# Performance work log

Measured on AMD Instinct MI355X. Metric: run time of the kernel, lower is better.

Reference implementation:

```python
import jax, jax.numpy as jnp
import numpy as np

H = 256           # hidden_size
D_IN = 4 * H      # 1024
D_K = 8 * H       # 2048
B, N = 8, 2048


def setup_inputs() -> dict:
    key = jax.random.key(0)
    ks = jax.random.split(key, 7)
    s_in = 1.0 / np.sqrt(D_IN)
    s_dk = 1.0 / np.sqrt(D_K)
    x = jax.random.normal(ks[0], (B, N, D_IN), dtype=jnp.float32)
    Wq = jax.random.uniform(ks[1], (D_IN, D_K), jnp.float32, -s_in, s_in)
    Wk = jax.random.uniform(ks[2], (D_IN, D_K), jnp.float32, -s_in, s_in)
    Wv = jax.random.uniform(ks[3], (D_IN, D_K), jnp.float32, -s_in, s_in)
    Wfc = jax.random.uniform(ks[4], (D_K, D_IN), jnp.float32, -s_dk, s_dk)
    bfc = jax.random.uniform(ks[5], (D_IN,), jnp.float32, -s_dk, s_dk)
    gamma = jnp.ones((D_IN,), jnp.float32)
    beta = jnp.zeros((D_IN,), jnp.float32)
    return {"x": x, "Wq": Wq, "Wk": Wk, "Wv": Wv, "Wfc": Wfc,
            "bfc": bfc, "gamma": gamma, "beta": beta}


def layer_norm(y, gamma, beta, eps=1e-5):
    mu = jnp.mean(y, axis=-1, keepdims=True)
    var = jnp.var(y, axis=-1, keepdims=True)
    return (y - mu) * jax.lax.rsqrt(var + eps) * gamma + beta


def reference(x, Wq, Wk, Wv, Wfc, bfc, gamma, beta):
    # Q/K/V projections: [B, N, D_K]
    q = jnp.einsum('bnd,dk->bnk', x, Wq)
    k = jnp.einsum('bnd,dk->bnk', x, Wk)
    v = jnp.einsum('bnd,dk->bnk', x, Wv)
    # NOTE: original module has NO 1/sqrt(d_k) scaling — keep it faithful.
    scores = jnp.einsum('bnk,bmk->bnm', q, k)           # [B, N, N]
    attn = jax.nn.softmax(scores, axis=-1)
    att_x = jnp.einsum('bnm,bmk->bnk', attn, v)          # [B, N, D_K]
    h = jax.nn.relu(jnp.einsum('bnk,kd->bnd', att_x, Wfc) + bfc)
    return layer_norm(x + h, gamma, beta)
```

## Files before the change

kernel.cpp:

```cpp
#include <hip/hip_runtime.h>
#include <stdint.h>


#define DEVI __device__ __forceinline__

typedef uint16_t u16;
typedef _Float16 f16x8 __attribute__((ext_vector_type(8)));
typedef float f32x4 __attribute__((ext_vector_type(4)));

DEVI u16 f2h(float f) {
  union { _Float16 h; u16 u; } v;
  v.h = (_Float16)f;
  return v.u;
}
DEVI float h2f(u16 x) {
  union { _Float16 h; u16 u; } v;
  v.u = x;
  return (float)v.h;
}

DEVI void gload_lds16(const void* g, void* lds) {
  __builtin_amdgcn_global_load_lds(
      (const __attribute__((address_space(1))) void*)g,
      (__attribute__((address_space(3))) void*)lds, 16, 0, 0);
}

#define GATE_S(N) do { asm volatile("s_waitcnt vmcnt(" #N ")" ::: "memory"); \
                       __builtin_amdgcn_s_barrier(); } while (0)
#define LGKM0 do { asm volatile("s_waitcnt lgkmcnt(0)" ::: "memory"); \
                   __builtin_amdgcn_sched_barrier(0); } while (0)

template <int EPI>
__global__ __launch_bounds__(512, 2) void gemm8x(
    const u16* __restrict__ A, const u16* __restrict__ B, void* __restrict__ C,
    int K, int lda, int ldb, int ldc,
    long aZ, long bZ, long cZ,
    const float* __restrict__ bias, const float* __restrict__ xres)
{
  __shared__ u16 lds[EPI == 3 ? 256 * 264 : 2 * 32768];
  char* ldsB = (char*)lds;
  const int tid = threadIdx.x;
  const int bz = blockIdx.z;

  const int gx = gridDim.x;
  int fl = blockIdx.y * gx + blockIdx.x;
  const int cpx = (gx * gridDim.y) >> 3;
  fl = (fl & 7) * cpx + (fl >> 3);
  const int bx = fl % gx, by = fl / gx;

  const u16* Ab = A + (long)bz * aZ + (long)(by * 256) * lda;
  const u16* Bb = B + (long)bz * bZ + (long)(bx * 256) * ldb;

  const int wid = tid >> 6, lane = tid & 63;
  const int wm = wid >> 2, wn = wid & 3;
  const int l15 = lane & 15;

  int aBase[2][2]; long aoff[2][2];
  int bBase[2][2]; long boff[2][2];
#pragma unroll
  for (int h = 0; h < 2; ++h) {
#pragma unroll
    for (int j = 0; j < 2; ++j) {
      const int s = wid * 2 + j;
      int rs = (s < 8) ? (64 * h + s * 8) : (128 + 64 * h + (s - 8) * 8);
      aBase[h][j] = rs * 128;
      {
        const int d = rs * 128 + lane * 16;
        const int dl = d ^ (((d >> 7) & 7) << 4);
        aoff[h][j] = (long)(dl >> 7) * (lda * 2) + (dl & 127);
      }
      rs = 64 * (s >> 2) + 32 * h + (s & 3) * 8;
      bBase[h][j] = 32768 + rs * 128;
      {
        const int d = rs * 128 + lane * 16;
        const int dl = d ^ (((d >> 7) & 7) << 4);
        boff[h][j] = (long)(dl >> 7) * (ldb * 2) + (dl & 127);
      }
    }
  }

  const int swz = (lane & 7) << 4;
  const int ko0 = ((lane >> 4) * 16) ^ swz;
  const int ko1 = (64 + (lane >> 4) * 16) ^ swz;

  f32x4 acc[8][4] = {};

  auto STAGE_A = [&](int t, int h) {
    char* dst = ldsB + (t & 1) * 65536;
    const long kB = (long)t * 128;
#pragma unroll
    for (int j = 0; j < 2; ++j)
      gload_lds16((const char*)Ab + aoff[h][j] + kB, dst + aBase[h][j]);
  };
  auto STAGE_B = [&](int t, int h) {
    char* dst = ldsB + (t & 1) * 65536;
    const long kB = (long)t * 128;
#pragma unroll
    for (int j = 0; j < 2; ++j)
      gload_lds16((const char*)Bb + boff[h][j] + kB, dst + bBase[h][j]);
  };
  auto RD_A = [&](const char* base, int mh, f16x8* dst) {
#pragma unroll
    for (int m = 0; m < 4; ++m) {
      const char* r = base + (wm * 128 + (mh * 4 + m) * 16 + l15) * 128;
      dst[2 * m] = *(const f16x8*)(r + ko0);
      dst[2 * m + 1] = *(const f16x8*)(r + ko1);
    }
  };
  auto RD_B = [&](const char* base, int nh, f16x8* dst) {
#pragma unroll
    for (int n = 0; n < 2; ++n) {
      const char* r = base + 32768 + (wn * 64 + (nh * 2 + n) * 16 + l15) * 128;
      dst[2 * n] = *(const f16x8*)(r + ko0);
      dst[2 * n + 1] = *(const f16x8*)(r + ko1);
    }
  };

  const int NT = K >> 6;
  const int NI = NT >> 1;
  const char* buf0 = ldsB;
  const char* buf1 = ldsB + 65536;

  STAGE_A(0, 0); STAGE_B(0, 0); STAGE_B(0, 1); STAGE_A(0, 1);
  STAGE_A(1, 0); STAGE_B(1, 0); STAGE_B(1, 1);

  for (int i = 0; i < NI; ++i) {
    const bool last = (i + 1 == NI);
    const int ta = 2 * i, tb = 2 * i + 1;
    f16x8 af[8], b0v[4], b1v[4];

    GATE_S(10);
    RD_A(buf0, 0, af); RD_B(buf0, 0, b0v);
    STAGE_A(tb, 1);
    LGKM0;
    __builtin_amdgcn_s_setprio(1);
#pragma unroll
    for (int ks = 0; ks < 2; ++ks)
#pragma unroll
      for (int m = 0; m < 4; ++m)
#pragma unroll
        for (int n = 0; n < 2; ++n)
          acc[m][n] = __builtin_amdgcn_mfma_f32_16x16x32_f16(
              af[2 * m + ks], b0v[2 * n + ks], acc[m][n], 0, 0, 0);
    __builtin_amdgcn_s_setprio(0);

    GATE_S(10);
    RD_B(buf0, 1, b1v);
    if (!last) STAGE_A(ta + 2, 0);
    LGKM0;
    __builtin_amdgcn_s_setprio(1);
#pragma unroll
    for (int ks = 0; ks < 2; ++ks)
#pragma unroll
      for (int m = 0; m < 4; ++m)
#pragma unroll
        for (int n = 0; n < 2; ++n)
          acc[m][n + 2] = __builtin_amdgcn_mfma_f32_16x16x32_f16(
              af[2 * m + ks], b1v[2 * n + ks], acc[m][n + 2], 0, 0, 0);
    __builtin_amdgcn_s_setprio(0);

    if (!last) GATE_S(10); else GATE_S(8);
    RD_A(buf0, 1, af);
    if (!last) STAGE_B(ta + 2, 0);
    LGKM0;
    __builtin_amdgcn_s_setprio(1);
#pragma unroll
    for (int ks = 0; ks < 2; ++ks)
#pragma unroll
      for (int m = 0; m < 4; ++m)
#pragma unroll
        for (int n = 0; n < 2; ++n)
          acc[m + 4][n] = __builtin_amdgcn_mfma_f32_16x16x32_f16(
              af[2 * m + ks], b0v[2 * n + ks], acc[m + 4][n], 0, 0, 0);
    __builtin_amdgcn_s_setprio(0);

    __builtin_amdgcn_s_barrier();
    if (!last) STAGE_B(ta + 2, 1);
    __builtin_amdgcn_s_setprio(1);
#pragma unroll
    for (int ks = 0; ks < 2; ++ks)
#pragma unroll
      for (int m = 0; m < 4; ++m)
#pragma unroll
        for (int n = 0; n < 2; ++n)
          acc[m + 4][n + 2] = __builtin_amdgcn_mfma_f32_16x16x32_f16(
              af[2 * m + ks], b1v[2 * n + ks], acc[m + 4][n + 2], 0, 0, 0);
    __builtin_amdgcn_s_setprio(0);

    if (!last) GATE_S(10); else GATE_S(4);
    RD_A(buf1, 0, af); RD_B(buf1, 0, b0v);
    if (!last) STAGE_A(ta + 2, 1);
    LGKM0;
    __builtin_amdgcn_s_setprio(1);
#pragma unroll
    for (int ks = 0; ks < 2; ++ks)
#pragma unroll
      for (int m = 0; m < 4; ++m)
#pragma unroll
        for (int n = 0; n < 2; ++n)
          acc[m][n] = __builtin_amdgcn_mfma_f32_16x16x32_f16(
              af[2 * m + ks], b0v[2 * n + ks], acc[m][n], 0, 0, 0);
    __builtin_amdgcn_s_setprio(0);

    if (!last) GATE_S(10); else GATE_S(2);
    RD_B(buf1, 1, b1v);
    if (!last) STAGE_A(tb + 2, 0);
    LGKM0;
    __builtin_amdgcn_s_setprio(1);
#pragma unroll
    for (int ks = 0; ks < 2; ++ks)
#pragma unroll
      for (int m = 0; m < 4; ++m)
#pragma unroll
        for (int n = 0; n < 2; ++n)
          acc[m][n + 2] = __builtin_amdgcn_mfma_f32_16x16x32_f16(
              af[2 * m + ks], b1v[2 * n + ks], acc[m][n + 2], 0, 0, 0);
    __builtin_amdgcn_s_setprio(0);

    if (!last) GATE_S(10); else GATE_S(0);
    RD_A(buf1, 1, af);
    if (!last) STAGE_B(tb + 2, 0);
    LGKM0;
    __builtin_amdgcn_s_setprio(1);
#pragma unroll
    for (int ks = 0; ks < 2; ++ks)
#pragma unroll
      for (int m = 0; m < 4; ++m)
#pragma unroll
        for (int n = 0; n < 2; ++n)
          acc[m + 4][n] = __builtin_amdgcn_mfma_f32_16x16x32_f16(
              af[2 * m + ks], b0v[2 * n + ks], acc[m + 4][n], 0, 0, 0);
    __builtin_amdgcn_s_setprio(0);

    __builtin_amdgcn_s_barrier();
    if (!last) STAGE_B(tb + 2, 1);
    __builtin_amdgcn_s_setprio(1);
#pragma unroll
    for (int ks = 0; ks < 2; ++ks)
#pragma unroll
      for (int m = 0; m < 4; ++m)
#pragma unroll
        for (int n = 0; n < 2; ++n)
          acc[m + 4][n + 2] = __builtin_amdgcn_mfma_f32_16x16x32_f16(
              af[2 * m + ks], b1v[2 * n + ks], acc[m + 4][n + 2], 0, 0, 0);
    __builtin_amdgcn_s_setprio(0);
  }

  const long cBase = (long)bz * cZ;
  const int rowBase = by * 256 + wm * 128;
  const int colBase = bx * 256 + wn * 64;

  if constexpr (EPI == 3) {
    u16* ldsT = (u16*)ldsB;
#pragma unroll
    for (int m = 0; m < 8; ++m) {
      const int row0 = wm * 128 + m * 16 + (lane >> 4) * 4;
#pragma unroll
      for (int n = 0; n < 4; ++n) {
        const int colL = wn * 64 + n * 16 + l15;
        ushort4 h;
        h.x = f2h(acc[m][n][0]); h.y = f2h(acc[m][n][1]);
        h.z = f2h(acc[m][n][2]); h.w = f2h(acc[m][n][3]);
        *(ushort4*)(ldsT + colL * 264 + row0) = h;
      }
    }
    __syncthreads();
    u16* vT = (u16*)C;
    const int rowBlk = by * 256;
    const long base2 = ((long)rowBlk >> 11) * 4194304L + (rowBlk & 2047);
#pragma unroll
    for (int p = 0; p < 16; ++p) {
      const int idx = tid + p * 512;
      const int colL = idx >> 5;
      const int ch = idx & 31;
      uint4 v = *(const uint4*)(ldsT + colL * 264 + ch * 8);
      *(uint4*)(vT + base2 + (long)(bx * 256 + colL) * 2048 + ch * 8) = v;
    }
  } else {
#pragma unroll
    for (int m = 0; m < 8; ++m) {
#pragma unroll
      for (int r = 0; r < 4; ++r) {
        const long row = rowBase + m * 16 + (lane >> 4) * 4 + r;
#pragma unroll
        for (int n = 0; n < 4; ++n) {
          const int col = colBase + n * 16 + l15;
          float v = acc[m][n][r];
          if constexpr (EPI == 0) {
            ((u16*)C)[cBase + row * ldc + col] = f2h(v);
          } else {
            v += bias[col];
            v = fmaxf(v, 0.0f);
            v += xres[row * (long)ldc + col];
            ((float*)C)[row * (long)ldc + col] = v;
          }
        }
      }
    }
  }
}

template <int EPI>
__global__ __launch_bounds__(256) void gemm_bt(
    const u16* __restrict__ A, const u16* __restrict__ B, void* __restrict__ C,
    int K, int lda, int ldb, int ldc,
    long aZ, long bZ, long cZ,
    const float* __restrict__ bias, const float* __restrict__ xres)
{
  __shared__ u16 sA[128 * 32];
  __shared__ u16 sB[128 * 32];
  const int tid = threadIdx.x;
  const int bz = blockIdx.z;
  const u16* Ab = A + (long)bz * aZ + (long)(blockIdx.y * 128) * lda;
  const u16* Bb = B + (long)bz * bZ + (long)(blockIdx.x * 128) * ldb;

  const int lane = tid & 63;
  const int wr = (tid >> 7) & 1;
  const int wc = (tid >> 6) & 1;
  const int l15 = lane & 15, l4 = lane >> 4;

  const int f0 = tid, f1 = tid + 256;
  const long ga0 = (long)(f0 >> 2) * lda + (f0 & 3) * 8;
  const long ga1 = (long)(f1 >> 2) * lda + (f1 & 3) * 8;
  const long gb0 = (long)(f0 >> 2) * ldb + (f0 & 3) * 8;
  const long gb1 = (long)(f1 >> 2) * ldb + (f1 & 3) * 8;
  u16* sAd0 = sA + (tid & ~63) * 8;
  u16* sAd1 = sA + 2048 + (tid & ~63) * 8;
  u16* sBd0 = sB + (tid & ~63) * 8;
  u16* sBd1 = sB + 2048 + (tid & ~63) * 8;

  f32x4 acc[4][4] = {};

  for (int k0 = 0; k0 < K; k0 += 32) {
    gload_lds16(Ab + ga0 + k0, sAd0);
    gload_lds16(Ab + ga1 + k0, sAd1);
    gload_lds16(Bb + gb0 + k0, sBd0);
    gload_lds16(Bb + gb1 + k0, sBd1);
    __syncthreads();
    f16x8 af[4], bf[4];
#pragma unroll
    for (int m = 0; m < 4; ++m)
      af[m] = *(const f16x8*)(sA + (wr * 64 + m * 16 + l15) * 32 + l4 * 8);
#pragma unroll
    for (int n = 0; n < 4; ++n)
      bf[n] = *(const f16x8*)(sB + (wc * 64 + n * 16 + l15) * 32 + l4 * 8);
#pragma unroll
    for (int m = 0; m < 4; ++m)
#pragma unroll
      for (int n = 0; n < 4; ++n)
        acc[m][n] = __builtin_amdgcn_mfma_f32_16x16x32_f16(af[m], bf[n], acc[m][n], 0, 0, 0);
    __syncthreads();
  }

  const long cBase = (long)bz * cZ;
  const int rowBase = blockIdx.y * 128 + wr * 64;
  const int colBase = blockIdx.x * 128 + wc * 64;

#pragma unroll
  for (int m = 0; m < 4; ++m) {
#pragma unroll
    for (int r = 0; r < 4; ++r) {
      const long row = rowBase + m * 16 + l4 * 4 + r;
#pragma unroll
      for (int n = 0; n < 4; ++n) {
        const int col = colBase + n * 16 + l15;
        float v = acc[m][n][r];
        if constexpr (EPI == 0) {
          ((u16*)C)[cBase + row * ldc + col] = f2h(v);
        } else if constexpr (EPI == 1) {
          ((float*)C)[cBase + row * ldc + col] = v;
        } else {
          v += bias[col];
          v = fmaxf(v, 0.0f);
          v += xres[row * (long)ldc + col];
          ((float*)C)[row * (long)ldc + col] = v;
        }
      }
    }
  }
}

__global__ __launch_bounds__(256) void softmax_rows16(u16* __restrict__ sc)
{
  const long row = blockIdx.x;
  u16* p = sc + row * 2048;
  const int tid = threadIdx.x;
  uint4 w = ((const uint4*)p)[tid];
  float e[8];
  e[0] = h2f(w.x & 0xffff); e[1] = h2f(w.x >> 16);
  e[2] = h2f(w.y & 0xffff); e[3] = h2f(w.y >> 16);
  e[4] = h2f(w.z & 0xffff); e[5] = h2f(w.z >> 16);
  e[6] = h2f(w.w & 0xffff); e[7] = h2f(w.w >> 16);
  float m = fmaxf(fmaxf(fmaxf(e[0], e[1]), fmaxf(e[2], e[3])),
                  fmaxf(fmaxf(e[4], e[5]), fmaxf(e[6], e[7])));
#pragma unroll
  for (int o = 32; o; o >>= 1) m = fmaxf(m, __shfl_xor(m, o));
  __shared__ float redm[4];
  if ((tid & 63) == 0) redm[tid >> 6] = m;
  __syncthreads();
  m = fmaxf(fmaxf(redm[0], redm[1]), fmaxf(redm[2], redm[3]));

  float s = 0.0f;
#pragma unroll
  for (int i = 0; i < 8; ++i) { e[i] = __expf(e[i] - m); s += e[i]; }
#pragma unroll
  for (int o = 32; o; o >>= 1) s += __shfl_xor(s, o);
  __shared__ float reds[4];
  if ((tid & 63) == 0) reds[tid >> 6] = s;
  __syncthreads();
  s = (reds[0] + reds[1]) + (reds[2] + reds[3]);
  const float inv = 1.0f / s;

  uint4 o;
  o.x = (uint32_t)f2h(e[0] * inv) | ((uint32_t)f2h(e[1] * inv) << 16);
  o.y = (uint32_t)f2h(e[2] * inv) | ((uint32_t)f2h(e[3] * inv) << 16);
  o.z = (uint32_t)f2h(e[4] * inv) | ((uint32_t)f2h(e[5] * inv) << 16);
  o.w = (uint32_t)f2h(e[6] * inv) | ((uint32_t)f2h(e[7] * inv) << 16);
  ((uint4*)p)[tid] = o;
}

__global__ __launch_bounds__(256) void softmax_rows(float* __restrict__ scores)
{
  const long row = blockIdx.x;
  const float* src = scores + row * 2048;
  const int tid = threadIdx.x;
  float4 a = ((const float4*)src)[tid];
  float4 b = ((const float4*)src)[tid + 256];
  float m = fmaxf(fmaxf(fmaxf(a.x, a.y), fmaxf(a.z, a.w)),
                  fmaxf(fmaxf(b.x, b.y), fmaxf(b.z, b.w)));
#pragma unroll
  for (int o = 32; o; o >>= 1) m = fmaxf(m, __shfl_xor(m, o));
  __shared__ float redm[4];
  if ((tid & 63) == 0) redm[tid >> 6] = m;
  __syncthreads();
  m = fmaxf(fmaxf(redm[0], redm[1]), fmaxf(redm[2], redm[3]));

  float e[8];
  e[0] = __expf(a.x - m); e[1] = __expf(a.y - m);
  e[2] = __expf(a.z - m); e[3] = __expf(a.w - m);
  e[4] = __expf(b.x - m); e[5] = __expf(b.y - m);
  e[6] = __expf(b.z - m); e[7] = __expf(b.w - m);
  float s = ((e[0] + e[1]) + (e[2] + e[3])) + ((e[4] + e[5]) + (e[6] + e[7]));
#pragma unroll
  for (int o = 32; o; o >>= 1) s += __shfl_xor(s, o);
  __shared__ float reds[4];
  if ((tid & 63) == 0) reds[tid >> 6] = s;
  __syncthreads();
  s = (reds[0] + reds[1]) + (reds[2] + reds[3]);
  const float inv = 1.0f / s;

  u16* dst = (u16*)scores + row * 4096;
  uint2 w0, w1;
  w0.x = (uint32_t)f2h(e[0] * inv) | ((uint32_t)f2h(e[1] * inv) << 16);
  w0.y = (uint32_t)f2h(e[2] * inv) | ((uint32_t)f2h(e[3] * inv) << 16);
  w1.x = (uint32_t)f2h(e[4] * inv) | ((uint32_t)f2h(e[5] * inv) << 16);
  w1.y = (uint32_t)f2h(e[6] * inv) | ((uint32_t)f2h(e[7] * inv) << 16);
  ((uint2*)dst)[tid] = w0;
  ((uint2*)dst)[tid + 256] = w1;
}

__global__ __launch_bounds__(256) void layernorm_rows(
    const float* __restrict__ y, const float* __restrict__ gamma,
    const float* __restrict__ beta, float* __restrict__ out)
{
  const long row = blockIdx.x;
  const int tid = threadIdx.x;
  float4 v = ((const float4*)(y + row * 1024))[tid];
  float s = (v.x + v.y) + (v.z + v.w);
  float q = (v.x * v.x + v.y * v.y) + (v.z * v.z + v.w * v.w);
#pragma unroll
  for (int o = 32; o; o >>= 1) { s += __shfl_xor(s, o); q += __shfl_xor(q, o); }
  __shared__ float rs[4], rq[4];
  if ((tid & 63) == 0) { rs[tid >> 6] = s; rq[tid >> 6] = q; }
  __syncthreads();
  s = (rs[0] + rs[1]) + (rs[2] + rs[3]);
  q = (rq[0] + rq[1]) + (rq[2] + rq[3]);
  const float mu = s * (1.0f / 1024.0f);
  const float var = q * (1.0f / 1024.0f) - mu * mu;
  const float rstd = rsqrtf(var + 1e-5f);
  float4 g = ((const float4*)gamma)[tid];
  float4 be = ((const float4*)beta)[tid];
  float4 o;
  o.x = (v.x - mu) * rstd * g.x + be.x;
  o.y = (v.y - mu) * rstd * g.y + be.y;
  o.z = (v.z - mu) * rstd * g.z + be.z;
  o.w = (v.w - mu) * rstd * g.w + be.w;
  __syncthreads();
  ((float4*)(out + row * 1024))[tid] = o;
}

__global__ __launch_bounds__(256) void cvt_f32_f16(
    const float* __restrict__ in, u16* __restrict__ out, long n4)
{
  const long stride = (long)gridDim.x * 256;
  for (long i = (long)blockIdx.x * 256 + threadIdx.x; i < n4; i += stride) {
    float4 v = ((const float4*)in)[i];
    uint2 p;
    p.x = (uint32_t)f2h(v.x) | ((uint32_t)f2h(v.y) << 16);
    p.y = (uint32_t)f2h(v.z) | ((uint32_t)f2h(v.w) << 16);
    ((uint2*)out)[i] = p;
  }
}

__global__ __launch_bounds__(256) void tw_f32(
    const float* __restrict__ in, u16* __restrict__ out, int R, int C)
{
  __shared__ float T[32][33];
  const int c0 = blockIdx.x * 32, r0 = blockIdx.y * 32;
  const int tx = threadIdx.x & 31, ty = threadIdx.x >> 5;
#pragma unroll
  for (int i = 0; i < 4; ++i)
    T[ty + i * 8][tx] = in[(long)(r0 + ty + i * 8) * C + c0 + tx];
  __syncthreads();
#pragma unroll
  for (int i = 0; i < 4; ++i)
    out[(long)(c0 + ty + i * 8) * R + r0 + tx] = f2h(T[tx][ty + i * 8]);
}

__global__ __launch_bounds__(256) void transpose_u16(
    const u16* __restrict__ in, u16* __restrict__ out, int R, int C)
{
  __shared__ u16 T[32][33];
  const long zo = (long)blockIdx.z * R * C;
  const int c0 = blockIdx.x * 32, r0 = blockIdx.y * 32;
  const int tx = threadIdx.x & 31, ty = threadIdx.x >> 5;
#pragma unroll
  for (int i = 0; i < 4; ++i)
    T[ty + i * 8][tx] = in[zo + (long)(r0 + ty + i * 8) * C + c0 + tx];
  __syncthreads();
#pragma unroll
  for (int i = 0; i < 4; ++i)
    out[zo + (long)(c0 + ty + i * 8) * R + r0 + tx] = T[tx][ty + i * 8];
}

extern "C" void kernel_launch(void* const* d_in, const int* in_sizes, int n_in,
                              void* d_out, int out_size, void* d_ws, size_t ws_size,
                              hipStream_t stream)
{
  const float* x     = (const float*)d_in[0];
  const float* Wq    = (const float*)d_in[1];
  const float* Wk    = (const float*)d_in[2];
  const float* Wv    = (const float*)d_in[3];
  const float* Wfc   = (const float*)d_in[4];
  const float* bfc   = (const float*)d_in[5];
  const float* gamma = (const float*)d_in[6];
  const float* beta  = (const float*)d_in[7];
  float* out = (float*)d_out;

  char* ws = (char*)d_ws;

  u16* wqkvT = (u16*)(ws + 0);
  u16* wfcT  = (u16*)(ws + 12582912);
  tw_f32<<<dim3(64, 32), 256, 0, stream>>>(Wq, wqkvT, 1024, 2048);
  tw_f32<<<dim3(64, 32), 256, 0, stream>>>(Wk, wqkvT + (long)2048 * 1024, 1024, 2048);
  tw_f32<<<dim3(64, 32), 256, 0, stream>>>(Wv, wqkvT + (long)2 * 2048 * 1024, 1024, 2048);
  tw_f32<<<dim3(32, 64), 256, 0, stream>>>(Wfc, wfcT, 2048, 1024);

  if (ws_size >= 251658240ULL) {
    u16*  q_   = (u16*)(ws + 16777216);
    u16*  k_   = (u16*)(ws + 83886080);
    u16*  vT   = (u16*)(ws + 150994944);
    u16*  sc16 = (u16*)(ws + 218103808);
    u16*  xb   = sc16;

    cvt_f32_f16<<<2048, 256, 0, stream>>>(x, xb, (long)16384 * 1024 / 4);

    gemm8x<0><<<dim3(8, 64, 2), 512, 0, stream>>>(
        xb, wqkvT, (void*)q_, 1024, 1024, 1024, 2048,
        0L, (long)2048 * 1024, (long)16384 * 2048, nullptr, nullptr);
    gemm8x<3><<<dim3(8, 64, 1), 512, 0, stream>>>(
        xb, wqkvT + (long)2 * 2048 * 1024, (void*)vT, 1024, 1024, 1024, 2048,
        0L, 0L, 0L, nullptr, nullptr);

    for (int c = 0; c < 2; ++c) {
      const u16* qc = q_ + (long)c * 1024 * 2048;
      gemm8x<0><<<dim3(8, 4, 8), 512, 0, stream>>>(
          qc, k_, (void*)sc16, 2048, 2048, 2048, 2048,
          (long)2048 * 2048, (long)2048 * 2048, (long)1024 * 2048, nullptr, nullptr);
      softmax_rows16<<<8192, 256, 0, stream>>>(sc16);
      gemm8x<0><<<dim3(8, 4, 8), 512, 0, stream>>>(
          sc16, vT, (void*)(q_ + (long)c * 1024 * 2048), 2048, 2048, 2048, 2048,
          (long)1024 * 2048, (long)2048 * 2048, (long)2048 * 2048, nullptr, nullptr);
    }

    gemm8x<2><<<dim3(4, 64, 1), 512, 0, stream>>>(
        q_, wfcT, (void*)out, 2048, 2048, 2048, 1024,
        0L, 0L, 0L, bfc, x);
  } else if (ws_size >= 109051904ULL) {
    u16*  xb2 = (u16*)(ws + 16777216);
    u16*  q2  = (u16*)(ws + 25165824);
    u16*  k2  = q2 + (long)2 * 2048 * 2048;
    u16*  v2  = q2 + (long)4 * 2048 * 2048;
    float* sc2 = (float*)(ws + 75497472);
    u16*  vT2   = k2;
    u16*  attx2 = q2;

    for (int p = 0; p < 4; ++p) {
      const float* xp = x + (long)p * 4096 * 1024;
      cvt_f32_f16<<<1024, 256, 0, stream>>>(xp, xb2, (long)4096 * 1024 / 4);
      for (int b = 0; b < 2; ++b)
        gemm_bt<0><<<dim3(16, 16, 3), 256, 0, stream>>>(
            xb2 + (long)b * 2048 * 1024, wqkvT, (void*)(q2 + (long)b * 2048 * 2048),
            1024, 1024, 1024, 2048,
            0L, (long)2048 * 1024, (long)2 * 2048 * 2048, nullptr, nullptr);
      gemm_bt<1><<<dim3(16, 16, 2), 256, 0, stream>>>(
          q2, k2, (void*)sc2, 2048, 2048, 2048, 2048,
          (long)2048 * 2048, (long)2048 * 2048, (long)2048 * 2048, nullptr, nullptr);
      softmax_rows<<<4096, 256, 0, stream>>>(sc2);
      transpose_u16<<<dim3(64, 64, 2), 256, 0, stream>>>(v2, vT2, 2048, 2048);
      gemm_bt<0><<<dim3(16, 16, 2), 256, 0, stream>>>(
          (const u16*)sc2, vT2, (void*)attx2, 2048, 4096, 2048, 2048,
          (long)2048 * 4096, (long)2048 * 2048, (long)2048 * 2048, nullptr, nullptr);
      gemm_bt<2><<<dim3(8, 32, 1), 256, 0, stream>>>(
          attx2, wfcT, (void*)(out + (long)p * 4096 * 1024), 2048, 2048, 2048, 1024,
          0L, 0L, 0L, bfc, xp);
    }
  } else {
    u16*  xb_b   = (u16*)(ws + 16777216);
    u16*  qkv_b  = (u16*)(ws + 20971520);
    u16*  q_b    = qkv_b;
    u16*  k_b    = qkv_b + (long)2048 * 2048;
    u16*  v_b    = qkv_b + (long)2 * 2048 * 2048;
    float* sc_b  = (float*)(ws + 46137344);
    u16*  vT_b   = k_b;
    u16*  attx_b = q_b;

    for (int b = 0; b < 8; ++b) {
      const float* x_b = x + (long)b * 2048 * 1024;
      cvt_f32_f16<<<512, 256, 0, stream>>>(x_b, xb_b, (long)2048 * 1024 / 4);
      gemm_bt<0><<<dim3(16, 16, 3), 256, 0, stream>>>(
          xb_b, wqkvT, (void*)qkv_b, 1024, 1024, 1024, 2048,
          0L, (long)2048 * 1024, (long)2048 * 2048, nullptr, nullptr);
      gemm_bt<1><<<dim3(16, 16, 1), 256, 0, stream>>>(
          q_b, k_b, (void*)sc_b, 2048, 2048, 2048, 2048,
          0L, 0L, 0L, nullptr, nullptr);
      softmax_rows<<<2048, 256, 0, stream>>>(sc_b);
      transpose_u16<<<dim3(64, 64, 1), 256, 0, stream>>>(v_b, vT_b, 2048, 2048);
      gemm_bt<0><<<dim3(16, 16, 1), 256, 0, stream>>>(
          (const u16*)sc_b, vT_b, (void*)attx_b, 2048, 4096, 2048, 2048,
          0L, 0L, 0L, nullptr, nullptr);
      gemm_bt<2><<<dim3(8, 16, 1), 256, 0, stream>>>(
          attx_b, wfcT, (void*)(out + (long)b * 2048 * 1024), 2048, 2048, 2048, 1024,
          0L, 0L, 0L, bfc, x_b);
    }
  }

  layernorm_rows<<<16384, 256, 0, stream>>>(out, gamma, beta, out);
}
```

Measured before the change: 592.2 us.

## Restructure GEMM main-loop sync: per-buffer vmcnt waits with split barriers

Replaces the per-quadrant combined vmcnt-wait-plus-barrier gates with a single vmcnt wait per half-iteration (per LDS buffer) and extra barriers placed around each MFMA quadrant. The aim is to stop stalling on outstanding global-to-LDS loads before every quadrant and to let loads overlap longer with compute. The cost is more barriers per iteration. It also risks racing on LDS reuse if the reduced vmcnt gating does not fully cover the data each quadrant reads. MFMA blocks are folded into a macro with no functional change.

```diff
diff --git a/kernel.cpp b/kernel.cpp
--- a/kernel.cpp
+++ b/kernel.cpp
@@ -25,10 +25,10 @@
       (__attribute__((address_space(3))) void*)lds, 16, 0, 0);
 }
 
-#define GATE_S(N) do { asm volatile("s_waitcnt vmcnt(" #N ")" ::: "memory"); \
-                       __builtin_amdgcn_s_barrier(); } while (0)
 #define LGKM0 do { asm volatile("s_waitcnt lgkmcnt(0)" ::: "memory"); \
                    __builtin_amdgcn_sched_barrier(0); } while (0)
+#define VMC(N) asm volatile("s_waitcnt vmcnt(" #N ")" ::: "memory")
+#define BAR()  __builtin_amdgcn_s_barrier()
 
 template <int EPI>
 __global__ __launch_bounds__(512, 2) void gemm8x(
@@ -116,6 +116,18 @@
     }
   };
 
+#define MFMA_QUAD(MO, NO, AV, BV)                                        \
+  __builtin_amdgcn_s_setprio(1);                                         \
+  _Pragma("unroll")                                                      \
+  for (int ks = 0; ks < 2; ++ks)                                         \
+    _Pragma("unroll")                                                    \
+    for (int m = 0; m < 4; ++m)                                          \
+      _Pragma("unroll")                                                  \
+      for (int n = 0; n < 2; ++n)                                        \
+        acc[m + MO][n + NO] = __builtin_amdgcn_mfma_f32_16x16x32_f16(    \
+            AV[2 * m + ks], BV[2 * n + ks], acc[m + MO][n + NO], 0, 0, 0); \
+  __builtin_amdgcn_s_setprio(0)
+
   const int NT = K >> 6;
   const int NI = NT >> 1;
   const char* buf0 = ldsB;
@@ -123,128 +135,69 @@
 
   STAGE_A(0, 0); STAGE_B(0, 0); STAGE_B(0, 1); STAGE_A(0, 1);
   STAGE_A(1, 0); STAGE_B(1, 0); STAGE_B(1, 1);
+  VMC(6);
+  BAR();
 
   for (int i = 0; i < NI; ++i) {
     const bool last = (i + 1 == NI);
     const int ta = 2 * i, tb = 2 * i + 1;
     f16x8 af[8], b0v[4], b1v[4];
 
-    GATE_S(10);
     RD_A(buf0, 0, af); RD_B(buf0, 0, b0v);
     STAGE_A(tb, 1);
+    BAR();
     LGKM0;
-    __builtin_amdgcn_s_setprio(1);
-#pragma unroll
-    for (int ks = 0; ks < 2; ++ks)
-#pragma unroll
-      for (int m = 0; m < 4; ++m)
-#pragma unroll
-        for (int n = 0; n < 2; ++n)
-          acc[m][n] = __builtin_amdgcn_mfma_f32_16x16x32_f16(
-              af[2 * m + ks], b0v[2 * n + ks], acc[m][n], 0, 0, 0);
-    __builtin_amdgcn_s_setprio(0);
-
-    GATE_S(10);
+    MFMA_QUAD(0, 0, af, b0v);
+    BAR();
+
     RD_B(buf0, 1, b1v);
     if (!last) STAGE_A(ta + 2, 0);
+    BAR();
     LGKM0;
-    __builtin_amdgcn_s_setprio(1);
-#pragma unroll
-    for (int ks = 0; ks < 2; ++ks)
-#pragma unroll
-      for (int m = 0; m < 4; ++m)
-#pragma unroll
-        for (int n = 0; n < 2; ++n)
-          acc[m][n + 2] = __builtin_amdgcn_mfma_f32_16x16x32_f16(
-              af[2 * m + ks], b1v[2 * n + ks], acc[m][n + 2], 0, 0, 0);
-    __builtin_amdgcn_s_setprio(0);
-
-    if (!last) GATE_S(10); else GATE_S(8);
+    MFMA_QUAD(0, 2, af, b1v);
+    BAR();
+
     RD_A(buf0, 1, af);
     if (!last) STAGE_B(ta + 2, 0);
+    BAR();
     LGKM0;
-    __builtin_amdgcn_s_setprio(1);
-#pragma unroll
-    for (int ks = 0; ks < 2; ++ks)
-#pragma unroll
-      for (int m = 0; m < 4; ++m)
-#pragma unroll
-        for (int n = 0; n < 2; ++n)
-          acc[m + 4][n] = __builtin_amdgcn_mfma_f32_16x16x32_f16(
-              af[2 * m + ks], b0v[2 * n + ks], acc[m + 4][n], 0, 0, 0);
-    __builtin_amdgcn_s_setprio(0);
-
-    __builtin_amdgcn_s_barrier();
+    MFMA_QUAD(4, 0, af, b0v);
+    BAR();
+
     if (!last) STAGE_B(ta + 2, 1);
-    __builtin_amdgcn_s_setprio(1);
-#pragma unroll
-    for (int ks = 0; ks < 2; ++ks)
-#pragma unroll
-      for (int m = 0; m < 4; ++m)
-#pragma unroll
-        for (int n = 0; n < 2; ++n)
-          acc[m + 4][n + 2] = __builtin_amdgcn_mfma_f32_16x16x32_f16(
-              af[2 * m + ks], b1v[2 * n + ks], acc[m + 4][n + 2], 0, 0, 0);
-    __builtin_amdgcn_s_setprio(0);
-
-    if (!last) GATE_S(10); else GATE_S(4);
+    BAR();
+    MFMA_QUAD(4, 2, af, b1v);
+    if (!last) VMC(6); else VMC(0);
+    BAR();
+
     RD_A(buf1, 0, af); RD_B(buf1, 0, b0v);
     if (!last) STAGE_A(ta + 2, 1);
+    BAR();
     LGKM0;
-    __builtin_amdgcn_s_setprio(1);
-#pragma unroll
-    for (int ks = 0; ks < 2; ++ks)
-#pragma unroll
-      for (int m = 0; m < 4; ++m)
-#pragma unroll
-        for (int n = 0; n < 2; ++n)
-          acc[m][n] = __builtin_amdgcn_mfma_f32_16x16x32_f16(
-              af[2 * m + ks], b0v[2 * n + ks], acc[m][n], 0, 0, 0);
-    __builtin_amdgcn_s_setprio(0);
-
-    if (!last) GATE_S(10); else GATE_S(2);
+    MFMA_QUAD(0, 0, af, b0v);
+    BAR();
+
     RD_B(buf1, 1, b1v);
     if (!last) STAGE_A(tb + 2, 0);
+    BAR();
     LGKM0;
-    __builtin_amdgcn_s_setprio(1);
-#pragma unroll
-    for (int ks = 0; ks < 2; ++ks)
-#pragma unroll
-      for (int m = 0; m < 4; ++m)
-#pragma unroll
-        for (int n = 0; n < 2; ++n)
-          acc[m][n + 2] = __builtin_amdgcn_mfma_f32_16x16x32_f16(
-              af[2 * m + ks], b1v[2 * n + ks], acc[m][n + 2], 0, 0, 0);
-    __builtin_amdgcn_s_setprio(0);
-
-    if (!last) GATE_S(10); else GATE_S(0);
+    MFMA_QUAD(0, 2, af, b1v);
+    BAR();
+
     RD_A(buf1, 1, af);
     if (!last) STAGE_B(tb + 2, 0);
+    BAR();
     LGKM0;
-    __builtin_amdgcn_s_setprio(1);
-#pragma unroll
-    for (int ks = 0; ks < 2; ++ks)
-#pragma unroll
-      for (int m = 0; m < 4; ++m)
-#pragma unroll
-        for (int n = 0; n < 2; ++n)
-          acc[m + 4][n] = __builtin_amdgcn_mfma_f32_16x16x32_f16(
-              af[2 * m + ks], b0v[2 * n + ks], acc[m + 4][n], 0, 0, 0);
-    __builtin_amdgcn_s_setprio(0);
-
-    __builtin_amdgcn_s_barrier();
+    MFMA_QUAD(4, 0, af, b0v);
+    BAR();
+
     if (!last) STAGE_B(tb + 2, 1);
-    __builtin_amdgcn_s_setprio(1);
-#pragma unroll
-    for (int ks = 0; ks < 2; ++ks)
-#pragma unroll
-      for (int m = 0; m < 4; ++m)
-#pragma unroll
-        for (int n = 0; n < 2; ++n)
-          acc[m + 4][n + 2] = __builtin_amdgcn_mfma_f32_16x16x32_f16(
-              af[2 * m + ks], b1v[2 * n + ks], acc[m + 4][n + 2], 0, 0, 0);
-    __builtin_amdgcn_s_setprio(0);
+    BAR();
+    MFMA_QUAD(4, 2, af, b1v);
+    if (!last) VMC(6);
+    BAR();
   }
+#undef MFMA_QUAD
 
   const long cBase = (long)bz * cZ;
   const int rowBase = by * 256 + wm * 128;
```

Measured after the change: 610.4 us. 1.03x slower.
